# Optimization experiments

Hardware: AMD Instinct MI355X
Metric: run time of the kernel (lower is better)

The kernel has to match this reference:

```python
import jax, jax.numpy as jnp
import numpy as np

N_HEADS = 4
NEG_SLOPE = 0.2  # DGL GATConv default leaky_relu slope


def setup_inputs() -> dict:
    key = jax.random.key(0)
    ks = jax.random.split(key, 12)
    N, E = 50000, 800000
    in_dim, time_dim, out_dim = 128, 128, 128
    d_head = out_dim // N_HEADS
    in_total = in_dim + time_dim
    h = jax.random.normal(ks[0], (N, in_dim), jnp.float32)
    time_tensor = jax.random.uniform(ks[1], (E,), jnp.float32)
    src = jax.random.randint(ks[2], (E,), 0, N, jnp.int32)
    dst = jax.random.randint(ks[3], (E,), 0, N, jnp.int32)
    # TimeEncoding: Linear(1, time_dim) with xavier weight, zero bias
    w_t = jax.random.normal(ks[4], (time_dim, 1), jnp.float32) * (6.0 / (1 + time_dim)) ** 0.5
    b_t = jnp.zeros((time_dim,), jnp.float32)
    # GATConv params
    W_fc = jax.random.normal(ks[5], (N_HEADS * d_head, in_total), jnp.float32) * (2.0 / in_total) ** 0.5
    attn_l = jax.random.normal(ks[6], (N_HEADS, d_head), jnp.float32) * 0.1
    attn_r = jax.random.normal(ks[7], (N_HEADS, d_head), jnp.float32) * 0.1
    W_res = jax.random.normal(ks[8], (N_HEADS * d_head, in_total), jnp.float32) * (2.0 / in_total) ** 0.5
    bias = jnp.zeros((N_HEADS * d_head,), jnp.float32)
    return {"h": h, "time_tensor": time_tensor, "src": src, "dst": dst,
            "num_nodes": N, "w_t": w_t, "b_t": b_t, "W_fc": W_fc,
            "attn_l": attn_l, "attn_r": attn_r, "W_res": W_res, "bias": bias}


def reference(h, time_tensor, src, dst, num_nodes, w_t, b_t, W_fc, attn_l, attn_r, W_res, bias):
    N = num_nodes
    E = src.shape[0]
    # Time encoding: cos(W t + b), per edge -> [E, time_dim]
    time_emb = jnp.cos(time_tensor[:, None] * w_t[:, 0][None, :] + b_t[None, :])
    # Mailbox mean of concat([src h, time_emb]) per dst node.
    # mean(concat) == concat(mean, mean), so sum the two halves separately.
    ones = jnp.ones((E,), h.dtype)
    deg = jax.ops.segment_sum(ones, dst, num_segments=N)  # [N]
    sum_h = jax.ops.segment_sum(h[src], dst, num_segments=N)       # [N, in_dim]
    sum_t = jax.ops.segment_sum(time_emb, dst, num_segments=N)     # [N, time_dim]
    inv_deg = 1.0 / jnp.maximum(deg, 1.0)
    h_time = jnp.concatenate([sum_h, sum_t], axis=1) * inv_deg[:, None]  # [N, in+time]
    # GATConv (eval mode, no dropout)
    d_head = W_fc.shape[0] // N_HEADS
    feat = (h_time @ W_fc.T).reshape(N, N_HEADS, d_head)  # [N,H,D]
    el = jnp.sum(feat * attn_l[None], axis=-1)  # [N,H]
    er = jnp.sum(feat * attn_r[None], axis=-1)  # [N,H]
    e = el[src] + er[dst]                        # [E,H]
    e = jnp.where(e > 0, e, NEG_SLOPE * e)
    # edge softmax over incoming edges of each dst node
    m = jax.ops.segment_max(e, dst, num_segments=N)  # [N,H]
    m = jnp.where(jnp.isfinite(m), m, 0.0)
    ex = jnp.exp(e - m[dst])
    denom = jax.ops.segment_sum(ex, dst, num_segments=N)
    a = ex / jnp.maximum(denom[dst], 1e-9)           # [E,H]
    rst = jax.ops.segment_sum(a[:, :, None] * feat[src], dst, num_segments=N)  # [N,H,D]
    res = (h_time @ W_res.T).reshape(N, N_HEADS, d_head)
    out = rst + res + bias.reshape(1, N_HEADS, d_head)
    out = jax.nn.elu(out)
    return out.reshape(N, -1)  # [N, out_dim]
```

## Files before the change

kernel.cpp:

```cpp
#include <hip/hip_runtime.h>
#include <math.h>

#define NH 4
#define NEG_SLOPE 0.2f
#define BKT_SHIFT 8
#define EPB 4096
#define CBLK 8192
#define TBLK 512
#define INV2PI 0.15915494309189535f
#define LOG2E  1.4426950408889634f

typedef __attribute__((ext_vector_type(8))) short bf16x8;
typedef __attribute__((ext_vector_type(4))) float f32x4;
typedef __attribute__((ext_vector_type(2))) float f32x2;

__device__ __forceinline__ float blo(unsigned u) { return __uint_as_float(u << 16); }
__device__ __forceinline__ float bhi(unsigned u) { return __uint_as_float(u & 0xFFFF0000u); }
__device__ __forceinline__ f32x2 mk2(float a, float b) { f32x2 r; r.x = a; r.y = b; return r; }
__device__ __forceinline__ f32x2 unpk(unsigned u) { return mk2(blo(u), bhi(u)); }
__device__ __forceinline__ unsigned short rne(float f) {
    unsigned u = __float_as_uint(f);
    u += 0x7FFFu + ((u >> 16) & 1u);
    return (unsigned short)(u >> 16);
}
__device__ __forceinline__ unsigned pack2(float a, float b) {
    return (unsigned)rne(a) | ((unsigned)rne(b) << 16);
}

__global__ __launch_bounds__(256) void k_prep(
    const float* __restrict__ h, unsigned* __restrict__ hbu, int n_pairs,
    const float* __restrict__ Wfc, const float* __restrict__ Wres,
    unsigned* __restrict__ wcat,
    const float* __restrict__ w_t, const float* __restrict__ b_t,
    unsigned* __restrict__ tbl,
    const int* __restrict__ dst, int* __restrict__ bkt_cnt, int E, int NB, int EB) {
    __shared__ int cnt[256];
    int tid = threadIdx.x;
    int t = blockIdx.x * blockDim.x + tid;
    if (t < n_pairs) {
        float2 v = ((const float2*)h)[t];
        hbu[t] = pack2(v.x, v.y);
    }
    if (t < 32768) {
        int col = t >> 7, kk = t & 127;
        const float* srcp = (col < 128) ? (Wfc + (size_t)col * 256)
                                        : (Wres + (size_t)(col - 128) * 256);
        float2 v = ((const float2*)srcp)[kk];
        int s  = col >> 6, ct = (col >> 4) & 3, r = col & 15;
        int ks = kk >> 4,  q  = (kk >> 2) & 3,  d = kk & 3;
        int w2i = ((s * 32 + ks * 4 + ct) << 8) + ((q * 16 + r) << 2) + d;
        wcat[w2i] = pack2(v.x, v.y);
    }
    if (blockIdx.x < (unsigned)EB) {
        cnt[tid] = 0;
        __syncthreads();
        int q0 = (blockIdx.x * CBLK) >> 2;
#pragma unroll
        for (int k = 0; k < CBLK / 1024; k++) {
            int qi = q0 + k * 256 + tid;
            int base = qi * 4;
            if (base + 3 < E) {
                int4 dd = ((const int4*)dst)[qi];
                atomicAdd(&cnt[dd.x >> BKT_SHIFT], 1);
                atomicAdd(&cnt[dd.y >> BKT_SHIFT], 1);
                atomicAdd(&cnt[dd.z >> BKT_SHIFT], 1);
                atomicAdd(&cnt[dd.w >> BKT_SHIFT], 1);
            } else {
                for (int e = base; e < E; e++) atomicAdd(&cnt[dst[e] >> BKT_SHIFT], 1);
            }
        }
        __syncthreads();
        if (tid < NB) {
            int c = cnt[tid];
            if (c) atomicAdd(bkt_cnt + tid, c);
        }
    }
    int tb = blockIdx.x - EB;
    if (tb >= 0 && tb < TBLK) {
        int idx = tb * 256 + tid;
        int j = idx >> 6, dp = idx & 63;
        int d0 = dp * 2;
        float tv = ((float)j + 0.5f) * (1.0f / 2048.0f);
        float w0 = w_t[d0] * INV2PI,     b0 = b_t[d0] * INV2PI;
        float w1 = w_t[d0 + 1] * INV2PI, b1 = b_t[d0 + 1] * INV2PI;
        tbl[idx] = pack2(__builtin_amdgcn_cosf(fmaf(tv, w0, b0)),
                         __builtin_amdgcn_cosf(fmaf(tv, w1, b1)));
    }
}

__global__ __launch_bounds__(256) void k_bktscan(
    const int* __restrict__ bkt_cnt, int* __restrict__ bkt_start,
    int* __restrict__ bkt_cursor, int* __restrict__ row_start,
    int NB, int E, int N) {
    __shared__ int wsum[4];
    int tid = threadIdx.x, lane = tid & 63, wid = tid >> 6;
    int v = (tid < NB) ? bkt_cnt[tid] : 0;
    int x = v;
#pragma unroll
    for (int off = 1; off < 64; off <<= 1) {
        int y = __shfl_up(x, off, 64);
        if (lane >= off) x += y;
    }
    if (lane == 63) wsum[wid] = x;
    __syncthreads();
    if (tid == 0) {
        int s = 0;
#pragma unroll
        for (int k = 0; k < 4; k++) { int tk = wsum[k]; wsum[k] = s; s += tk; }
    }
    __syncthreads();
    int excl = wsum[wid] + x - v;
    if (tid < NB) { bkt_start[tid] = excl; bkt_cursor[tid] = excl; }
    if (tid == 0) { bkt_start[NB] = E; row_start[N] = E; }
}

__global__ __launch_bounds__(256) void k_binscatter(
    const int* __restrict__ src, const int* __restrict__ dst,
    const float* __restrict__ tt, int* __restrict__ bkt_cursor,
    uint2* __restrict__ staged, int E, int NB) {
    __shared__ int cnt[1024];
    __shared__ int basep[1024];
    int e0 = blockIdx.x * EPB;
    int tid = threadIdx.x;
    for (int b = tid; b < NB; b += 256) cnt[b] = 0;
    __syncthreads();
#pragma unroll
    for (int k = 0; k < EPB / 256; k++) {
        int e = e0 + k * 256 + tid;
        if (e < E) atomicAdd(&cnt[dst[e] >> BKT_SHIFT], 1);
    }
    __syncthreads();
    for (int b = tid; b < NB; b += 256) {
        int c = cnt[b];
        basep[b] = (c > 0) ? atomicAdd(bkt_cursor + b, c) : 0;
        cnt[b] = 0;
    }
    __syncthreads();
#pragma unroll
    for (int k = 0; k < EPB / 256; k++) {
        int e = e0 + k * 256 + tid;
        if (e < E) {
            int d = dst[e];
            int b = d >> BKT_SHIFT;
            int r = atomicAdd(&cnt[b], 1);
            unsigned tq = min((unsigned)(tt[e] * 32768.0f), 32767u);
            staged[basep[b] + r] =
                make_uint2(((unsigned)src[e] << 15) | tq, (unsigned)(d & 255));
        }
    }
}

__global__ __launch_bounds__(256) void k_binsort(
    const uint2* __restrict__ staged, const int* __restrict__ bkt_start,
    int* __restrict__ row_start, unsigned* __restrict__ est, int N) {
    __shared__ int cnt[256];
    __shared__ int cur[256];
    __shared__ int wsum[4];
    int b = blockIdx.x;
    int n0 = b << BKT_SHIFT;
    int tid = threadIdx.x;
    cnt[tid] = 0;
    __syncthreads();
    int s0 = bkt_start[b], s1 = bkt_start[b + 1];
    for (int p = s0 + tid; p < s1; p += 256)
        atomicAdd(&cnt[staged[p].y], 1);
    __syncthreads();
    int lane = tid & 63, wid = tid >> 6;
    int v = cnt[tid];
    int x = v;
#pragma unroll
    for (int off = 1; off < 64; off <<= 1) {
        int y = __shfl_up(x, off, 64);
        if (lane >= off) x += y;
    }
    if (lane == 63) wsum[wid] = x;
    __syncthreads();
    if (tid == 0) {
        int s = 0;
#pragma unroll
        for (int k = 0; k < 4; k++) { int tk = wsum[k]; wsum[k] = s; s += tk; }
    }
    __syncthreads();
    int excl = s0 + wsum[wid] + x - v;
    cur[tid] = excl;
    if (n0 + tid < N) row_start[n0 + tid] = excl;
    __syncthreads();
    for (int p = s0 + tid; p < s1; p += 256) {
        uint2 vv = staged[p];
        int pos = atomicAdd(&cur[vv.y], 1);
        est[pos] = vv.x;
    }
}

__device__ __forceinline__ void agg_edge(unsigned u, float wgt, const char* __restrict__ hb,
                                         const char* __restrict__ tb, int i,
                                         f32x2* aH, f32x2* aT) {
    unsigned hoff = (u >> 15) << 8;
    unsigned toff = (u & 0x7FF0u) << 4;
    uint4 hv = *(const uint4*)(hb + hoff + i * 16);
    uint4 tv = *(const uint4*)(tb + toff + i * 16);
    f32x2 w2 = mk2(wgt, wgt);
    aH[0] = w2 * unpk(hv.x) + aH[0];
    aH[1] = w2 * unpk(hv.y) + aH[1];
    aH[2] = w2 * unpk(hv.z) + aH[2];
    aH[3] = w2 * unpk(hv.w) + aH[3];
    aT[0] = w2 * unpk(tv.x) + aT[0];
    aT[1] = w2 * unpk(tv.y) + aT[1];
    aT[2] = w2 * unpk(tv.z) + aT[2];
    aT[3] = w2 * unpk(tv.w) + aT[3];
}

__device__ __forceinline__ void attn_edge(unsigned u, bool valid, const char* __restrict__ fb,
                                          int i, int hd, const char* __restrict__ elb,
                                          float erh, f32x2* acc, float& den) {
    unsigned off = (u >> 15) << 8;
    float elh = *(const float*)(elb + (off >> 4) + (hd << 2));
    uint4 fv = *(const uint4*)(fb + off + i * 16);
    float w = elh + erh; w = w > 0.f ? w : NEG_SLOPE * w;
    float ex = valid ? __builtin_amdgcn_exp2f(w) : 0.f;
    f32x2 ex2 = mk2(ex, ex);
    acc[0] = ex2 * unpk(fv.x) + acc[0];
    acc[1] = ex2 * unpk(fv.y) + acc[1];
    acc[2] = ex2 * unpk(fv.z) + acc[2];
    acc[3] = ex2 * unpk(fv.w) + acc[3];
    den += ex;
}

__global__ __launch_bounds__(256) void k_agg(
    const unsigned* __restrict__ hbu, const unsigned* __restrict__ tbl,
    const unsigned* __restrict__ est, const int* __restrict__ row_start,
    unsigned* __restrict__ htu, int N) {
    int tid = threadIdx.x;
    int i = tid & 15;
    int n = blockIdx.x * 16 + (tid >> 4);
    if (n >= N) return;
    const char* hb = (const char*)hbu;
    const char* tb = (const char*)tbl;
    int rs = row_start[n], re = row_start[n + 1];
    f32x2 aH[4] = {}, aT[4] = {};
    int e = rs;
    int nfull = (re - rs) >> 2;
    for (int j = 0; j < nfull; j++, e += 4) {
        unsigned u0 = est[e];
        unsigned u1 = est[e + 1];
        unsigned u2 = est[e + 2];
        unsigned u3 = est[e + 3];
        agg_edge(u0, 1.0f, hb, tb, i, aH, aT);
        agg_edge(u1, 1.0f, hb, tb, i, aH, aT);
        agg_edge(u2, 1.0f, hb, tb, i, aH, aT);
        agg_edge(u3, 1.0f, hb, tb, i, aH, aT);
    }
    if (e < re) {
        unsigned u0 = est[e];
        bool v1 = e + 1 < re, v2 = e + 2 < re;
        unsigned u1 = v1 ? est[e + 1] : u0;
        unsigned u2 = v2 ? est[e + 2] : u0;
        agg_edge(u0, 1.0f, hb, tb, i, aH, aT);
        agg_edge(u1, v1 ? 1.0f : 0.0f, hb, tb, i, aH, aT);
        agg_edge(u2, v2 ? 1.0f : 0.0f, hb, tb, i, aH, aT);
    }
    int deg = re - rs;
    float idg = (deg > 0) ? 1.0f / (float)deg : 1.0f;
    uint4* ht4 = (uint4*)htu;
    uint4 oh, ot;
    oh.x = pack2(aH[0].x * idg, aH[0].y * idg);
    oh.y = pack2(aH[1].x * idg, aH[1].y * idg);
    oh.z = pack2(aH[2].x * idg, aH[2].y * idg);
    oh.w = pack2(aH[3].x * idg, aH[3].y * idg);
    ot.x = pack2(aT[0].x * idg, aT[0].y * idg);
    ot.y = pack2(aT[1].x * idg, aT[1].y * idg);
    ot.z = pack2(aT[2].x * idg, aT[2].y * idg);
    ot.w = pack2(aT[3].x * idg, aT[3].y * idg);
    ht4[(size_t)n * 32 + i]      = oh;
    ht4[(size_t)n * 32 + 16 + i] = ot;
}

__global__ __launch_bounds__(256) void k_gemm(
    const unsigned short* __restrict__ ht, const unsigned* __restrict__ wcat,
    unsigned short* __restrict__ feat, float* __restrict__ res_out, int N) {
    __shared__ __align__(16) unsigned short As[64 * 264];
    int tid = threadIdx.x;
    int row0 = blockIdx.x * 64;
    const uint4* src4 = (const uint4*)ht;
    for (int idx = tid; idx < 64 * 32; idx += 256) {
        int rl = idx >> 5, c16 = idx & 31;
        int gr = row0 + rl; if (gr >= N) gr = N - 1;
        uint4 v = src4[(size_t)gr * 32 + c16];
        *(uint4*)(As + rl * 264 + c16 * 8) = v;
    }
    __syncthreads();
    int wave = tid >> 6, lane = tid & 63;
    int r = lane & 15, q = lane >> 4;
    int colbase = wave * 64;
    const bf16x8* bbase = (const bf16x8*)wcat + (size_t)wave * 2048 + lane;
    const unsigned short* abase = As + r * 264 + q * 8;
    f32x4 acc[4][4] = {};
#pragma unroll
    for (int ks = 0; ks < 8; ks++) {
        bf16x8 a[4], b[4];
#pragma unroll
        for (int rt = 0; rt < 4; rt++)
            a[rt] = *(const bf16x8*)(abase + rt * (16 * 264) + ks * 32);
#pragma unroll
        for (int ct = 0; ct < 4; ct++)
            b[ct] = bbase[(ks * 4 + ct) * 64];
#pragma unroll
        for (int rt = 0; rt < 4; rt++)
#pragma unroll
            for (int ct = 0; ct < 4; ct++)
                acc[rt][ct] = __builtin_amdgcn_mfma_f32_16x16x32_bf16(a[rt], b[ct], acc[rt][ct], 0, 0, 0);
    }
    bool featw = (colbase < 128);
#pragma unroll
    for (int rt = 0; rt < 4; rt++) {
        int rb = row0 + rt * 16 + q * 4;
#pragma unroll
        for (int ct = 0; ct < 4; ct++) {
            int col = colbase + ct * 16 + r;
#pragma unroll
            for (int reg = 0; reg < 4; reg++) {
                int row = rb + reg;
                if (row >= N) continue;
                float v = acc[rt][ct][reg];
                if (featw) feat[(size_t)row * 128 + col] = rne(v);
                else       res_out[(size_t)row * 128 + (col - 128)] = v;
            }
        }
    }
}

__global__ void k_el_er(const unsigned* __restrict__ featu,
                        const float* __restrict__ attn_l, const float* __restrict__ attn_r,
                        float* __restrict__ el, float* __restrict__ er, int NH4) {
    int t = blockIdx.x * blockDim.x + threadIdx.x;
    if (t >= NH4) return;
    int n = t >> 2, hd = t & 3;
    const unsigned* f = featu + (size_t)n * 64 + hd * 16;
    const float2* al = (const float2*)(attn_l + hd * 32);
    const float2* ar = (const float2*)(attn_r + hd * 32);
    float sl = 0.f, sr = 0.f;
#pragma unroll
    for (int i = 0; i < 16; i++) {
        unsigned u = f[i];
        float f0 = blo(u), f1 = bhi(u);
        float2 a = al[i], b = ar[i];
        sl = fmaf(f0, a.x, fmaf(f1, a.y, sl));
        sr = fmaf(f0, b.x, fmaf(f1, b.y, sr));
    }
    el[t] = sl * LOG2E;
    er[t] = sr * LOG2E;
}

__global__ __launch_bounds__(256) void k_attn(
    const unsigned* __restrict__ est, const int* __restrict__ row_start,
    const float* __restrict__ el, const float* __restrict__ er,
    const unsigned* __restrict__ featu, const float* __restrict__ bias,
    float* __restrict__ out, int N) {
    int tid = threadIdx.x;
    int i = tid & 15;
    int hd = i >> 2;
    int n = blockIdx.x * 16 + (tid >> 4);
    if (n >= N) return;
    int rs = row_start[n], re = row_start[n + 1];
    float erh = er[(size_t)n * 4 + hd];
    const char* fb = (const char*)featu;
    const char* elb = (const char*)el;
    f32x2 acc[4] = {};
    float den = 0.f;
    int e = rs;
    int nfull = (re - rs) >> 2;
    for (int j = 0; j < nfull; j++, e += 4) {
        unsigned u0 = est[e];
        unsigned u1 = est[e + 1];
        unsigned u2 = est[e + 2];
        unsigned u3 = est[e + 3];
        attn_edge(u0, true, fb, i, hd, elb, erh, acc, den);
        attn_edge(u1, true, fb, i, hd, elb, erh, acc, den);
        attn_edge(u2, true, fb, i, hd, elb, erh, acc, den);
        attn_edge(u3, true, fb, i, hd, elb, erh, acc, den);
    }
    if (e < re) {
        unsigned u0 = est[e];
        bool v1 = e + 1 < re, v2 = e + 2 < re;
        unsigned u1 = v1 ? est[e + 1] : u0;
        unsigned u2 = v2 ? est[e + 2] : u0;
        attn_edge(u0, true, fb, i, hd, elb, erh, acc, den);
        attn_edge(u1, v1, fb, i, hd, elb, erh, acc, den);
        attn_edge(u2, v2, fb, i, hd, elb, erh, acc, den);
    }
    float id = 1.0f / fmaxf(den, 1e-9f);
    float* op = out + (size_t)n * 128 + i * 8;
    const float* bp = bias + i * 8;
    float4 o0 = ((const float4*)op)[0], o1 = ((const float4*)op)[1];
    float4 b0 = ((const float4*)bp)[0], b1 = ((const float4*)bp)[1];
    float4 r0, r1;
    r0.x = fmaf(acc[0].x, id, o0.x + b0.x);
    r0.y = fmaf(acc[0].y, id, o0.y + b0.y);
    r0.z = fmaf(acc[1].x, id, o0.z + b0.z);
    r0.w = fmaf(acc[1].y, id, o0.w + b0.w);
    r1.x = fmaf(acc[2].x, id, o1.x + b1.x);
    r1.y = fmaf(acc[2].y, id, o1.y + b1.y);
    r1.z = fmaf(acc[3].x, id, o1.z + b1.z);
    r1.w = fmaf(acc[3].y, id, o1.w + b1.w);
    r0.x = r0.x > 0.f ? r0.x : (__expf(r0.x) - 1.0f);
    r0.y = r0.y > 0.f ? r0.y : (__expf(r0.y) - 1.0f);
    r0.z = r0.z > 0.f ? r0.z : (__expf(r0.z) - 1.0f);
    r0.w = r0.w > 0.f ? r0.w : (__expf(r0.w) - 1.0f);
    r1.x = r1.x > 0.f ? r1.x : (__expf(r1.x) - 1.0f);
    r1.y = r1.y > 0.f ? r1.y : (__expf(r1.y) - 1.0f);
    r1.z = r1.z > 0.f ? r1.z : (__expf(r1.z) - 1.0f);
    r1.w = r1.w > 0.f ? r1.w : (__expf(r1.w) - 1.0f);
    ((float4*)op)[0] = r0;
    ((float4*)op)[1] = r1;
}

extern "C" void kernel_launch(void* const* d_in, const int* in_sizes, int n_in,
                              void* d_out, int out_size, void* d_ws, size_t ws_size,
                              hipStream_t stream) {
    const float* h     = (const float*)d_in[0];
    const float* tt    = (const float*)d_in[1];
    const int*   src   = (const int*)d_in[2];
    const int*   dst   = (const int*)d_in[3];
    const float* w_t   = (const float*)d_in[5];
    const float* b_t   = (const float*)d_in[6];
    const float* W_fc  = (const float*)d_in[7];
    const float* al    = (const float*)d_in[8];
    const float* ar    = (const float*)d_in[9];
    const float* W_res = (const float*)d_in[10];
    const float* bias  = (const float*)d_in[11];

    int N = in_sizes[0] / 128;
    int E = in_sizes[1];
    int NB = (N + 255) >> BKT_SHIFT;
    int EB = (E + CBLK - 1) / CBLK;

    char* ws = (char*)d_ws;
    size_t off = 0;
    auto alloc = [&](size_t bytes) { void* p = ws + off; off = (off + bytes + 15) & ~(size_t)15; return p; };
    unsigned* htu     = (unsigned*)alloc((size_t)N * 128 * 4);
    unsigned* hbu     = (unsigned*)alloc((size_t)N * 64 * 4);
    unsigned* featu   = (unsigned*)alloc((size_t)N * 64 * 4);
    unsigned* wcat    = (unsigned*)alloc(32768 * 4);
    unsigned* tbl     = (unsigned*)alloc((size_t)2048 * 64 * 4);
    float*    el      = (float*)alloc((size_t)N * NH * 4);
    float*    er      = (float*)alloc((size_t)N * NH * 4);
    int*      row_st  = (int*)alloc((size_t)(N + 1) * 4);
    int*      bkt_cur = (int*)alloc((size_t)NB * 4);
    int*      bkt_cnt = (int*)alloc((size_t)NB * 4);
    int*      bkt_sta = (int*)alloc((size_t)(NB + 1) * 4);
    unsigned* est     = (unsigned*)alloc((size_t)E * 4);
    uint2*    staged  = (uint2*)featu;

    hipMemsetAsync(bkt_cnt, 0, (size_t)NB * 4, stream);

    int prep_n = N * 64;
    hipLaunchKernelGGL(k_prep, dim3((prep_n + 255) / 256), dim3(256), 0, stream,
                       h, hbu, prep_n, W_fc, W_res, wcat, w_t, b_t, tbl,
                       dst, bkt_cnt, E, NB, EB);
    hipLaunchKernelGGL(k_bktscan, dim3(1), dim3(256), 0, stream,
                       bkt_cnt, bkt_sta, bkt_cur, row_st, NB, E, N);
    hipLaunchKernelGGL(k_binscatter, dim3((E + EPB - 1) / EPB), dim3(256), 0, stream,
                       src, dst, tt, bkt_cur, staged, E, NB);
    hipLaunchKernelGGL(k_binsort, dim3(NB), dim3(256), 0, stream,
                       staged, bkt_sta, row_st, est, N);
    hipLaunchKernelGGL(k_agg, dim3((N + 15) / 16), dim3(256), 0, stream,
                       hbu, tbl, est, row_st, htu, N);
    hipLaunchKernelGGL(k_gemm, dim3((N + 63) / 64), dim3(256), 0, stream,
                       (const unsigned short*)htu, wcat,
                       (unsigned short*)featu, (float*)d_out, N);
    hipLaunchKernelGGL(k_el_er, dim3((N * NH + 255) / 256), dim3(256), 0, stream,
                       featu, al, ar, el, er, N * NH);
    hipLaunchKernelGGL(k_attn, dim3((N + 15) / 16), dim3(256), 0, stream,
                       est, row_st, el, er, featu, bias, (float*)d_out, N);
}
```

Measured before the change: 240.5 us.

## Shrink GEMM row tile to 16 and load A fragments directly from global

The GEMM kernel drops the LDS staging of a 64-row A tile and its barrier. Each block now handles 16 rows, and every wave reads its bf16 A fragment straight from global memory. This gives 4x more blocks, fewer accumulator registers and possibly higher occupancy. In exchange, each A tile is read by all four waves from global or cache, and the B weights are reloaded by 4x more blocks, so weight traffic and reuse get worse.

```diff
diff --git a/kernel.cpp b/kernel.cpp
--- a/kernel.cpp
+++ b/kernel.cpp
@@ -278,53 +278,37 @@
 __global__ __launch_bounds__(256) void k_gemm(
     const unsigned short* __restrict__ ht, const unsigned* __restrict__ wcat,
     unsigned short* __restrict__ feat, float* __restrict__ res_out, int N) {
-    __shared__ __align__(16) unsigned short As[64 * 264];
-    int tid = threadIdx.x;
-    int row0 = blockIdx.x * 64;
-    const uint4* src4 = (const uint4*)ht;
-    for (int idx = tid; idx < 64 * 32; idx += 256) {
-        int rl = idx >> 5, c16 = idx & 31;
-        int gr = row0 + rl; if (gr >= N) gr = N - 1;
-        uint4 v = src4[(size_t)gr * 32 + c16];
-        *(uint4*)(As + rl * 264 + c16 * 8) = v;
-    }
-    __syncthreads();
+    int tid = threadIdx.x;
     int wave = tid >> 6, lane = tid & 63;
     int r = lane & 15, q = lane >> 4;
+    int row0 = blockIdx.x * 16;
     int colbase = wave * 64;
+    int gr = row0 + r; if (gr >= N) gr = N - 1;
+    const bf16x8* a_base = (const bf16x8*)ht + (size_t)gr * 32;
     const bf16x8* bbase = (const bf16x8*)wcat + (size_t)wave * 2048 + lane;
-    const unsigned short* abase = As + r * 264 + q * 8;
-    f32x4 acc[4][4] = {};
+    f32x4 acc[4] = {};
 #pragma unroll
     for (int ks = 0; ks < 8; ks++) {
-        bf16x8 a[4], b[4];
-#pragma unroll
-        for (int rt = 0; rt < 4; rt++)
-            a[rt] = *(const bf16x8*)(abase + rt * (16 * 264) + ks * 32);
+        bf16x8 a = a_base[ks * 4 + q];
+        bf16x8 b[4];
 #pragma unroll
         for (int ct = 0; ct < 4; ct++)
             b[ct] = bbase[(ks * 4 + ct) * 64];
 #pragma unroll
-        for (int rt = 0; rt < 4; rt++)
-#pragma unroll
-            for (int ct = 0; ct < 4; ct++)
-                acc[rt][ct] = __builtin_amdgcn_mfma_f32_16x16x32_bf16(a[rt], b[ct], acc[rt][ct], 0, 0, 0);
+        for (int ct = 0; ct < 4; ct++)
+            acc[ct] = __builtin_amdgcn_mfma_f32_16x16x32_bf16(a, b[ct], acc[ct], 0, 0, 0);
     }
     bool featw = (colbase < 128);
 #pragma unroll
-    for (int rt = 0; rt < 4; rt++) {
-        int rb = row0 + rt * 16 + q * 4;
-#pragma unroll
-        for (int ct = 0; ct < 4; ct++) {
-            int col = colbase + ct * 16 + r;
-#pragma unroll
-            for (int reg = 0; reg < 4; reg++) {
-                int row = rb + reg;
-                if (row >= N) continue;
-                float v = acc[rt][ct][reg];
-                if (featw) feat[(size_t)row * 128 + col] = rne(v);
-                else       res_out[(size_t)row * 128 + (col - 128)] = v;
-            }
+    for (int ct = 0; ct < 4; ct++) {
+        int col = colbase + ct * 16 + r;
+#pragma unroll
+        for (int reg = 0; reg < 4; reg++) {
+            int row = row0 + q * 4 + reg;
+            if (row >= N) continue;
+            float v = acc[ct][reg];
+            if (featw) feat[(size_t)row * 128 + col] = rne(v);
+            else       res_out[(size_t)row * 128 + (col - 128)] = v;
         }
     }
 }
@@ -465,7 +449,7 @@
                        staged, bkt_sta, row_st, est, N);
     hipLaunchKernelGGL(k_agg, dim3((N + 15) / 16), dim3(256), 0, stream,
                        hbu, tbl, est, row_st, htu, N);
-    hipLaunchKernelGGL(k_gemm, dim3((N + 63) / 64), dim3(256), 0, stream,
+    hipLaunchKernelGGL(k_gemm, dim3((N + 15) / 16), dim3(256), 0, stream,
                        (const unsigned short*)htu, wcat,
                        (unsigned short*)featu, (float*)d_out, N);
     hipLaunchKernelGGL(k_el_er, dim3((N * NH + 255) / 256), dim3(256), 0, stream,
```

Measured after the change: 246.4 us. +2.4%, slower.
